# Performance work log

Measured on AMD Instinct MI355X. Metric: run time of the kernel, lower is better.

Reference implementation:

```python
import jax, jax.numpy as jnp
import numpy as np

B = 2          # number of point clouds (batch vector has B blocks)
N_PER = 16384  # points per cloud
F = 32         # input feature dim
D = 3          # coordinate dim
RATIO = 0.25
R = 0.2        # ball-query radius
K = 64         # max_neighbors
H1 = 64        # MLP hidden
COUT = 128     # MLP output
M = int(N_PER * RATIO)  # centroids per cloud


def setup_inputs() -> dict:
    key = jax.random.key(0)
    k0, k1, k2, k3 = jax.random.split(key, 4)
    x = jax.random.normal(k0, (B * N_PER, F), jnp.float32)
    pos = jax.random.uniform(k1, (B * N_PER, D), jnp.float32)
    batch = jnp.repeat(jnp.arange(B), N_PER)
    W1 = jax.random.normal(k2, (F + D, H1), jnp.float32) / np.sqrt(F + D)
    b1 = jnp.zeros((H1,), jnp.float32)
    W2 = jax.random.normal(k3, (H1, COUT), jnp.float32) / np.sqrt(H1)
    b2 = jnp.zeros((COUT,), jnp.float32)
    return {"x": x, "pos": pos, "batch": batch, "W1": W1, "b1": b1, "W2": W2, "b2": b2}


def _fps(pos_b):
    """Iterative farthest point sampling: (N_PER, D) -> (M,) indices."""
    d0 = jnp.sum((pos_b - pos_b[0]) ** 2, axis=-1)  # start at point 0

    def body(d, _):
        i = jnp.argmax(d)
        d = jnp.minimum(d, jnp.sum((pos_b - pos_b[i]) ** 2, axis=-1))
        return d, i

    _, idxs = jax.lax.scan(body, d0, None, length=M - 1)
    return jnp.concatenate([jnp.zeros((1,), idxs.dtype), idxs])


def _set_abstraction(x_b, pos_b, W1, b1, W2, b2):
    idx = _fps(pos_b)            # (M,)
    pc = pos_b[idx]              # centroid positions (M, D)
    # ball query: squared distances centroids -> all points, capped at K neighbors
    d2 = jnp.sum((pc[:, None, :] - pos_b[None, :, :]) ** 2, axis=-1)  # (M, N_PER)
    neg = jnp.where(d2 <= R * R, -d2, -jnp.inf)
    vals, nbr = jax.lax.top_k(neg, K)        # K nearest within radius
    valid = vals > -jnp.inf                  # (M, K)
    xj = x_b[nbr]                            # (M, K, F)
    pj = pos_b[nbr]                          # (M, K, D)
    # faithful to source: msg = pos_j - pos_i / r  (note: pos_i/r, not (pos_j-pos_i)/r)
    msg = jnp.concatenate([xj, pj - pc[:, None, :] / R], axis=-1)  # (M, K, F+D)
    h = jax.nn.relu(msg @ W1 + b1) @ W2 + b2                       # (M, K, COUT)
    h = jnp.where(valid[:, :, None], h, -jnp.inf)
    out = jnp.max(h, axis=1)                 # max aggregation over neighbors
    out = jnp.where(jnp.isfinite(out), out, 0.0)
    return out, pc


def reference(x, pos, batch, W1, b1, W2, b2):
    xb = x.reshape(B, N_PER, F)
    pb = pos.reshape(B, N_PER, D)
    out, pc = jax.vmap(lambda xx, pp: _set_abstraction(xx, pp, W1, b1, W2, b2))(xb, pb)
    batch_out = jnp.repeat(jnp.arange(B, dtype=batch.dtype), M)
    return out.reshape(B * M, COUT), pc.reshape(B * M, D), batch_out
```

## Files before the change

kernel.cpp:

```cpp
#include <hip/hip_runtime.h>
#include <hip/hip_bf16.h>

#define NPTS 16384
#define MCENT 4096
#define BCLD 2
#define FDIM 32
#define H1DIM 64
#define CODIM 128
#define KNBR 64
#define R2CUT 0.04f

__device__ __forceinline__ float d2e(float ax, float ay, float az,
                                     float bx, float by, float bz) {
  float dx = __fsub_rn(ax, bx);
  float dy = __fsub_rn(ay, by);
  float dz = __fsub_rn(az, bz);
  return __fadd_rn(__fadd_rn(__fmul_rn(dx, dx), __fmul_rn(dy, dy)), __fmul_rn(dz, dz));
}

__device__ __forceinline__ int spread3(int v) {
  return ((v & 4) << 4) | ((v & 2) << 2) | (v & 1);
}
__device__ __forceinline__ int cell_of(float x, float y, float z) {
  int cx = min(7, (int)(x * 8.0f));
  int cy = min(7, (int)(y * 8.0f));
  int cz = min(7, (int)(z * 8.0f));
  return (spread3(cx) << 2) | (spread3(cy) << 1) | spread3(cz);
}

#define DPP_LEXMAX_STEP(bb, nn, ctrl)                                          \
  do {                                                                         \
    unsigned _ob = (unsigned)__builtin_amdgcn_update_dpp(0, (int)(bb), ctrl,   \
                                                         0xf, 0xf, false);     \
    unsigned _on = (unsigned)__builtin_amdgcn_update_dpp(0, (int)(nn), ctrl,   \
                                                         0xf, 0xf, false);     \
    bool _t = (_ob > (bb)) || (_ob == (bb) && _on > (nn));                     \
    (bb) = _t ? _ob : (bb);                                                    \
    (nn) = _t ? _on : (nn);                                                    \
  } while (0)

__device__ __forceinline__ int rdlane(int v, int l) {
  return __builtin_amdgcn_readlane(v, l);
}
__device__ __forceinline__ float rdlanef(float v, int l) {
  return __int_as_float(__builtin_amdgcn_readlane(__float_as_int(v), l));
}

__global__ __launch_bounds__(1024) void fps_kernel(const float* __restrict__ pos,
                                                   int* __restrict__ fps_idx,
                                                   float4* __restrict__ ws_sorted) {
  const int b = blockIdx.x;
  const float* P = pos + (size_t)b * NPTS * 3;
  float4* S = ws_sorted + (size_t)b * NPTS;
  const int tid = threadIdx.x;
  const int lane = tid & 63;
  const int wave = tid >> 6;

  __shared__ int hist[512];
  __shared__ int offs[512];
  __shared__ unsigned long long skey[2][16];
  __shared__ float4 spos[2][16];
  __shared__ int winners[MCENT];

  if (tid < 512) hist[tid] = 0;
  __syncthreads();
#pragma unroll 4
  for (int j = 0; j < 16; ++j) {
    int i = tid + j * 1024;
    float x = P[3 * i + 0], y = P[3 * i + 1], z = P[3 * i + 2];
    atomicAdd(&hist[cell_of(x, y, z)], 1);
  }
  __syncthreads();
  if (tid < 64) {
    int base = tid * 8;
    int loc[8];
    int run = 0;
#pragma unroll
    for (int k = 0; k < 8; ++k) { loc[k] = run; run += hist[base + k]; }
    int inc = run;
#pragma unroll
    for (int off = 1; off < 64; off <<= 1) {
      int o = __shfl_up(inc, off);
      if (tid >= off) inc += o;
    }
    int ex = inc - run;
#pragma unroll
    for (int k = 0; k < 8; ++k) offs[base + k] = ex + loc[k];
  }
  __syncthreads();
#pragma unroll 4
  for (int j = 0; j < 16; ++j) {
    int i = tid + j * 1024;
    float x = P[3 * i + 0], y = P[3 * i + 1], z = P[3 * i + 2];
    int p = atomicAdd(&offs[cell_of(x, y, z)], 1);
    S[p] = make_float4(x, y, z, __int_as_float(i));
  }
  __syncthreads();

  float px[16], py[16], pz[16], d[16];
  unsigned nidx[16];
  const float x0 = P[0], y0 = P[1], z0 = P[2];
  float bxm, bxM, bym, byM, bzm, bzM;
  unsigned tb = 0u, tn = 0u;
  float tx = 0.f, ty = 0.f, tz = 0.f;
#pragma unroll
  for (int j = 0; j < 16; ++j) {
    float4 v = S[tid * 16 + j];
    px[j] = v.x; py[j] = v.y; pz[j] = v.z;
    nidx[j] = ~(unsigned)__float_as_int(v.w);
    float dj = d2e(v.x, v.y, v.z, x0, y0, z0);
    d[j] = dj;
    if (j == 0) {
      bxm = v.x; bxM = v.x; bym = v.y; byM = v.y; bzm = v.z; bzM = v.z;
    } else {
      bxm = fminf(bxm, v.x); bxM = fmaxf(bxM, v.x);
      bym = fminf(bym, v.y); byM = fmaxf(byM, v.y);
      bzm = fminf(bzm, v.z); bzM = fmaxf(bzM, v.z);
    }
    unsigned db = __float_as_uint(dj);
    unsigned nj = nidx[j];
    bool t = (db > tb) || (db == tb && nj > tn);
    tb = t ? db : tb; tn = t ? nj : tn;
    tx = t ? v.x : tx; ty = t ? v.y : ty; tz = t ? v.z : tz;
  }

  if (tid == 0) winners[0] = 0;

  bool wavedirty = true;
  unsigned cwb = 0u, cwn = 0u;
  float cwx = 0.f, cwy = 0.f, cwz = 0.f;

  for (int m = 1; m < MCENT; ++m) {
    const int par = m & 1;

    if (wavedirty) {
      unsigned bb = tb, nn = tn;
      DPP_LEXMAX_STEP(bb, nn, 0x111);
      DPP_LEXMAX_STEP(bb, nn, 0x112);
      DPP_LEXMAX_STEP(bb, nn, 0x114);
      DPP_LEXMAX_STEP(bb, nn, 0x118);
      DPP_LEXMAX_STEP(bb, nn, 0x142);
      DPP_LEXMAX_STEP(bb, nn, 0x143);
      cwb = (unsigned)rdlane((int)bb, 63);
      cwn = (unsigned)rdlane((int)nn, 63);
      unsigned long long own = __ballot(tb == cwb && tn == cwn);
      int ol = (int)__ffsll(own) - 1;
      cwx = rdlanef(tx, ol);
      cwy = rdlanef(ty, ol);
      cwz = rdlanef(tz, ol);
    }
    if (lane == 0) {
      skey[par][wave] = ((unsigned long long)cwb << 32) | (unsigned long long)cwn;
      spos[par][wave] = make_float4(cwx, cwy, cwz, 0.0f);
    }
    __syncthreads();

    unsigned rb, rn;
    unsigned sb0 = 0u, sn0 = 0u;
    {
      unsigned bb = 0u, nn = 0u;
      if (lane < 16) {
        unsigned long long kk = skey[par][lane];
        bb = (unsigned)(kk >> 32);
        nn = (unsigned)kk;
        sb0 = bb; sn0 = nn;
        DPP_LEXMAX_STEP(bb, nn, 0x111);
        DPP_LEXMAX_STEP(bb, nn, 0x112);
        DPP_LEXMAX_STEP(bb, nn, 0x114);
        DPP_LEXMAX_STEP(bb, nn, 0x118);
      }
      rb = (unsigned)rdlane((int)bb, 15);
      rn = (unsigned)rdlane((int)nn, 15);
    }
    unsigned long long wm = __ballot(lane < 16 && sb0 == rb && sn0 == rn);
    int ws = (int)__ffsll(wm) - 1;
    float4 wp = spos[par][ws];
    if (tid == 0) winners[m] = (int)(~rn);

    float ex = fmaxf(fmaxf(bxm - wp.x, wp.x - bxM), 0.0f);
    float ey = fmaxf(fmaxf(bym - wp.y, wp.y - byM), 0.0f);
    float ez = fmaxf(fmaxf(bzm - wp.z, wp.z - bzM), 0.0f);
    float lb = (ex * ex + ey * ey + ez * ez) * 0.999f;
    bool mydirty = lb < __uint_as_float(tb);
    if (mydirty) {
      unsigned nb = 0u, nn2 = 0u;
      float nx = 0.f, ny = 0.f, nz = 0.f;
#pragma unroll
      for (int j = 0; j < 16; ++j) {
        float dj = fminf(d[j], d2e(px[j], py[j], pz[j], wp.x, wp.y, wp.z));
        d[j] = dj;
        unsigned db = __float_as_uint(dj);
        unsigned nj = nidx[j];
        bool t = (db > nb) || (db == nb && nj > nn2);
        nb = t ? db : nb; nn2 = t ? nj : nn2;
        nx = t ? px[j] : nx; ny = t ? py[j] : ny; nz = t ? pz[j] : nz;
      }
      tb = nb; tn = nn2; tx = nx; ty = ny; tz = nz;
    }
    wavedirty = (__ballot(mydirty) != 0ULL);
  }

  __syncthreads();
  for (int i = tid; i < MCENT; i += 1024) fps_idx[b * MCENT + i] = winners[i];
}

__global__ __launch_bounds__(256) void ballq_kernel(const float* __restrict__ pos,
                                                    const int* __restrict__ fps_idx,
                                                    int* __restrict__ nbr,
                                                    float* __restrict__ out_pc,
                                                    float* __restrict__ out_batch) {
  const int wave = threadIdx.x >> 6;
  const int lane = threadIdx.x & 63;
  const int c = blockIdx.x * 4 + wave;
  const int b = c >> 12;
  const float* P = pos + (size_t)b * NPTS * 3;

  const int ci = fps_idx[c];
  const float cx = P[3 * ci + 0];
  const float cy = P[3 * ci + 1];
  const float cz = P[3 * ci + 2];
  if (lane == 0) {
    out_pc[3 * c + 0] = cx;
    out_pc[3 * c + 1] = cy;
    out_pc[3 * c + 2] = cz;
    out_batch[c] = (float)b;
  }

  __shared__ unsigned long long list[4][1024];
  __shared__ int cnt[4];
  if (lane == 0) cnt[wave] = 0;

  for (int i = lane; i < NPTS; i += 64) {
    const float qx = P[3 * i + 0];
    const float qy = P[3 * i + 1];
    const float qz = P[3 * i + 2];
    const float dd = d2e(cx, cy, cz, qx, qy, qz);
    if (dd <= R2CUT) {
      int p = atomicAdd(&cnt[wave], 1);
      if (p < 1024)
        list[wave][p] = ((unsigned long long)__float_as_uint(dd) << 32)
                      | (unsigned long long)(unsigned)i;
    }
  }
  __syncthreads();

  int n = cnt[wave];
  if (n > 1024) n = 1024;

  unsigned long long loc[16];
#pragma unroll
  for (int k = 0; k < 16; ++k) {
    int i = lane + k * 64;
    loc[k] = (i < n) ? list[wave][i] : ~0ULL;
  }
  unsigned long long mv = loc[0];
#pragma unroll
  for (int k = 1; k < 16; ++k)
    if (loc[k] < mv) mv = loc[k];

  int myout = -1;
  for (int s = 0; s < 64; ++s) {
    unsigned long long wmin = mv;
#pragma unroll
    for (int off = 32; off >= 1; off >>= 1) {
      unsigned long long o = __shfl_xor(wmin, off);
      if (o < wmin) wmin = o;
    }
    if (lane == s) myout = (wmin == ~0ULL) ? -1 : (int)(unsigned)wmin;
    if (mv == wmin && wmin != ~0ULL) {
#pragma unroll
      for (int k = 0; k < 16; ++k)
        if (loc[k] == wmin) loc[k] = ~0ULL;
      mv = loc[0];
#pragma unroll
      for (int k = 1; k < 16; ++k)
        if (loc[k] < mv) mv = loc[k];
    }
  }
  nbr[c * KNBR + lane] = myout;
}

__global__ __launch_bounds__(256) void mlp_kernel(const float* __restrict__ pos,
                                                  const float* __restrict__ x,
                                                  const int* __restrict__ fps_idx,
                                                  const int* __restrict__ nbr,
                                                  const float* __restrict__ W1,
                                                  const float* __restrict__ b1,
                                                  const float* __restrict__ W2,
                                                  const float* __restrict__ b2,
                                                  float* __restrict__ out) {
  const int c = blockIdx.x;
  const int b = c >> 12;
  const float* P = pos + (size_t)b * NPTS * 3;
  const float* X = x + (size_t)b * NPTS * FDIM;

  __shared__ float W1s[35 * 64];
  __shared__ float W2s[64 * 128];
  __shared__ float b1s[64];
  __shared__ float b2s[128];
  __shared__ float h1s[64][64];
  __shared__ float pmax[2][128];
  __shared__ int validk[64];

  const int tid = threadIdx.x;
  for (int i = tid; i < 35 * 64; i += 256) W1s[i] = W1[i];
  for (int i = tid; i < 64 * 128; i += 256) W2s[i] = W2[i];
  if (tid < 64) b1s[tid] = b1[tid];
  else if (tid < 192) b2s[tid - 64] = b2[tid - 64];

  const int ci = fps_idx[c];
  const float c5x = P[3 * ci + 0] / 0.2f;
  const float c5y = P[3 * ci + 1] / 0.2f;
  const float c5z = P[3 * ci + 2] / 0.2f;

  const int k = tid >> 2, q = tid & 3;
  const int nk = nbr[c * KNBR + k];
  if (q == 0) validk[k] = (nk >= 0) ? 1 : 0;
  const int nkc = (nk < 0) ? 0 : nk;

  float msg[35];
  const float4* Xr = (const float4*)(X + (size_t)nkc * FDIM);
#pragma unroll
  for (int i4 = 0; i4 < 8; ++i4) {
    float4 v = Xr[i4];
    msg[i4 * 4 + 0] = v.x; msg[i4 * 4 + 1] = v.y;
    msg[i4 * 4 + 2] = v.z; msg[i4 * 4 + 3] = v.w;
  }
  msg[32] = P[3 * nkc + 0] - c5x;
  msg[33] = P[3 * nkc + 1] - c5y;
  msg[34] = P[3 * nkc + 2] - c5z;

  __syncthreads();

  float acc[16];
#pragma unroll
  for (int h = 0; h < 16; ++h) acc[h] = b1s[q * 16 + h];
#pragma unroll
  for (int i = 0; i < 35; ++i) {
    const float m = msg[i];
    const float4* wrow = (const float4*)&W1s[i * 64 + q * 16];
#pragma unroll
    for (int j4 = 0; j4 < 4; ++j4) {
      float4 w = wrow[j4];
      acc[j4 * 4 + 0] += m * w.x;
      acc[j4 * 4 + 1] += m * w.y;
      acc[j4 * 4 + 2] += m * w.z;
      acc[j4 * 4 + 3] += m * w.w;
    }
  }
#pragma unroll
  for (int h = 0; h < 16; ++h) h1s[k][q * 16 + h] = fmaxf(acc[h], 0.0f);
  __syncthreads();

  const int ch = tid & 127, half = tid >> 7;
  float w2r[64];
#pragma unroll
  for (int i = 0; i < 64; ++i) w2r[i] = W2s[i * 128 + ch];

  float mx = -INFINITY;
  for (int k2 = half * 32; k2 < half * 32 + 32; ++k2) {
    if (!validk[k2]) continue;
    float s = b2s[ch];
    const float4* hr = (const float4*)h1s[k2];
#pragma unroll
    for (int i4 = 0; i4 < 16; ++i4) {
      float4 h4 = hr[i4];
      s += h4.x * w2r[i4 * 4 + 0] + h4.y * w2r[i4 * 4 + 1]
         + h4.z * w2r[i4 * 4 + 2] + h4.w * w2r[i4 * 4 + 3];
    }
    mx = fmaxf(mx, s);
  }
  pmax[half][ch] = mx;
  __syncthreads();

  if (tid < 128) {
    float m2 = fmaxf(pmax[0][tid], pmax[1][tid]);
    out[(size_t)c * CODIM + tid] = (m2 > -INFINITY) ? m2 : 0.0f;
  }
}

extern "C" void kernel_launch(void* const* d_in, const int* in_sizes, int n_in,
                              void* d_out, int out_size, void* d_ws, size_t ws_size,
                              hipStream_t stream) {
  const float* x   = (const float*)d_in[0];
  const float* pos = (const float*)d_in[1];
  const float* W1  = (const float*)d_in[3];
  const float* b1  = (const float*)d_in[4];
  const float* W2  = (const float*)d_in[5];
  const float* b2  = (const float*)d_in[6];
  float* out = (float*)d_out;

  int* fps_idx = (int*)d_ws;
  int* nbr     = (int*)d_ws + BCLD * MCENT;
  float4* ws_sorted = (float4*)nbr;

  float* out_pc    = out + (size_t)BCLD * MCENT * CODIM;
  float* out_batch = out_pc + (size_t)BCLD * MCENT * 3;

  hipLaunchKernelGGL(fps_kernel, dim3(BCLD), dim3(1024), 0, stream, pos, fps_idx, ws_sorted);
  hipLaunchKernelGGL(ballq_kernel, dim3(BCLD * MCENT / 4), dim3(256), 0, stream,
                     pos, fps_idx, nbr, out_pc, out_batch);
  hipLaunchKernelGGL(mlp_kernel, dim3(BCLD * MCENT), dim3(256), 0, stream,
                     pos, x, fps_idx, nbr, W1, b1, W2, b2, out);
}
```

Before: 7.694 ms.

## Halve FPS block size with 32 points per thread and per-half bounding boxes

```diff
diff --git a/kernel.cpp b/kernel.cpp
--- a/kernel.cpp
+++ b/kernel.cpp
@@ -46,9 +46,9 @@
   return __int_as_float(__builtin_amdgcn_readlane(__float_as_int(v), l));
 }
 
-__global__ __launch_bounds__(1024) void fps_kernel(const float* __restrict__ pos,
-                                                   int* __restrict__ fps_idx,
-                                                   float4* __restrict__ ws_sorted) {
+__global__ __launch_bounds__(512, 2) void fps_kernel(const float* __restrict__ pos,
+                                                     int* __restrict__ fps_idx,
+                                                     float4* __restrict__ ws_sorted) {
   const int b = blockIdx.x;
   const float* P = pos + (size_t)b * NPTS * 3;
   float4* S = ws_sorted + (size_t)b * NPTS;
@@ -58,15 +58,15 @@
 
   __shared__ int hist[512];
   __shared__ int offs[512];
-  __shared__ unsigned long long skey[2][16];
-  __shared__ float4 spos[2][16];
+  __shared__ unsigned long long skey[2][8];
+  __shared__ float4 spos[2][8];
   __shared__ int winners[MCENT];
 
-  if (tid < 512) hist[tid] = 0;
+  hist[tid] = 0;
   __syncthreads();
 #pragma unroll 4
-  for (int j = 0; j < 16; ++j) {
-    int i = tid + j * 1024;
+  for (int j = 0; j < 32; ++j) {
+    int i = tid + j * 512;
     float x = P[3 * i + 0], y = P[3 * i + 1], z = P[3 * i + 2];
     atomicAdd(&hist[cell_of(x, y, z)], 1);
   }
@@ -89,39 +89,47 @@
   }
   __syncthreads();
 #pragma unroll 4
-  for (int j = 0; j < 16; ++j) {
-    int i = tid + j * 1024;
+  for (int j = 0; j < 32; ++j) {
+    int i = tid + j * 512;
     float x = P[3 * i + 0], y = P[3 * i + 1], z = P[3 * i + 2];
     int p = atomicAdd(&offs[cell_of(x, y, z)], 1);
     S[p] = make_float4(x, y, z, __int_as_float(i));
   }
   __syncthreads();
 
-  float px[16], py[16], pz[16], d[16];
-  unsigned nidx[16];
+  float px[32], py[32], pz[32], d[32];
+  unsigned nidx[32];
+  float bxm[2], bxM[2], bym[2], byM[2], bzm[2], bzM[2];
+  unsigned hb[2], hn[2];
+  float hx[2], hy[2], hz[2];
   const float x0 = P[0], y0 = P[1], z0 = P[2];
-  float bxm, bxM, bym, byM, bzm, bzM;
-  unsigned tb = 0u, tn = 0u;
-  float tx = 0.f, ty = 0.f, tz = 0.f;
-#pragma unroll
-  for (int j = 0; j < 16; ++j) {
-    float4 v = S[tid * 16 + j];
-    px[j] = v.x; py[j] = v.y; pz[j] = v.z;
-    nidx[j] = ~(unsigned)__float_as_int(v.w);
-    float dj = d2e(v.x, v.y, v.z, x0, y0, z0);
-    d[j] = dj;
-    if (j == 0) {
-      bxm = v.x; bxM = v.x; bym = v.y; byM = v.y; bzm = v.z; bzM = v.z;
-    } else {
-      bxm = fminf(bxm, v.x); bxM = fmaxf(bxM, v.x);
-      bym = fminf(bym, v.y); byM = fmaxf(byM, v.y);
-      bzm = fminf(bzm, v.z); bzM = fmaxf(bzM, v.z);
-    }
-    unsigned db = __float_as_uint(dj);
-    unsigned nj = nidx[j];
-    bool t = (db > tb) || (db == tb && nj > tn);
-    tb = t ? db : tb; tn = t ? nj : tn;
-    tx = t ? v.x : tx; ty = t ? v.y : ty; tz = t ? v.z : tz;
+#pragma unroll
+  for (int h = 0; h < 2; ++h) {
+    unsigned nb = 0u, nn2 = 0u;
+    float nx = 0.f, ny = 0.f, nz = 0.f;
+#pragma unroll
+    for (int jj = 0; jj < 16; ++jj) {
+      const int j = h * 16 + jj;
+      float4 v = S[tid * 32 + j];
+      px[j] = v.x; py[j] = v.y; pz[j] = v.z;
+      nidx[j] = ~(unsigned)__float_as_int(v.w);
+      float dj = d2e(v.x, v.y, v.z, x0, y0, z0);
+      d[j] = dj;
+      if (jj == 0) {
+        bxm[h] = v.x; bxM[h] = v.x; bym[h] = v.y; byM[h] = v.y;
+        bzm[h] = v.z; bzM[h] = v.z;
+      } else {
+        bxm[h] = fminf(bxm[h], v.x); bxM[h] = fmaxf(bxM[h], v.x);
+        bym[h] = fminf(bym[h], v.y); byM[h] = fmaxf(byM[h], v.y);
+        bzm[h] = fminf(bzm[h], v.z); bzM[h] = fmaxf(bzM[h], v.z);
+      }
+      unsigned db = __float_as_uint(dj);
+      unsigned nj = nidx[j];
+      bool t = (db > nb) || (db == nb && nj > nn2);
+      nb = t ? db : nb; nn2 = t ? nj : nn2;
+      nx = t ? v.x : nx; ny = t ? v.y : ny; nz = t ? v.z : nz;
+    }
+    hb[h] = nb; hn[h] = nn2; hx[h] = nx; hy[h] = ny; hz[h] = nz;
   }
 
   if (tid == 0) winners[0] = 0;
@@ -132,6 +140,14 @@
 
   for (int m = 1; m < MCENT; ++m) {
     const int par = m & 1;
+
+    unsigned tb = hb[0], tn = hn[0];
+    float tx = hx[0], ty = hy[0], tz = hz[0];
+    {
+      bool t = (hb[1] > tb) || (hb[1] == tb && hn[1] > tn);
+      tb = t ? hb[1] : tb; tn = t ? hn[1] : tn;
+      tx = t ? hx[1] : tx; ty = t ? hy[1] : ty; tz = t ? hz[1] : tz;
+    }
 
     if (wavedirty) {
       unsigned bb = tb, nn = tn;
@@ -159,7 +175,7 @@
     unsigned sb0 = 0u, sn0 = 0u;
     {
       unsigned bb = 0u, nn = 0u;
-      if (lane < 16) {
+      if (lane < 8) {
         unsigned long long kk = skey[par][lane];
         bb = (unsigned)(kk >> 32);
         nn = (unsigned)kk;
@@ -167,41 +183,45 @@
         DPP_LEXMAX_STEP(bb, nn, 0x111);
         DPP_LEXMAX_STEP(bb, nn, 0x112);
         DPP_LEXMAX_STEP(bb, nn, 0x114);
-        DPP_LEXMAX_STEP(bb, nn, 0x118);
       }
-      rb = (unsigned)rdlane((int)bb, 15);
-      rn = (unsigned)rdlane((int)nn, 15);
-    }
-    unsigned long long wm = __ballot(lane < 16 && sb0 == rb && sn0 == rn);
+      rb = (unsigned)rdlane((int)bb, 7);
+      rn = (unsigned)rdlane((int)nn, 7);
+    }
+    unsigned long long wm = __ballot(lane < 8 && sb0 == rb && sn0 == rn);
     int ws = (int)__ffsll(wm) - 1;
     float4 wp = spos[par][ws];
     if (tid == 0) winners[m] = (int)(~rn);
 
-    float ex = fmaxf(fmaxf(bxm - wp.x, wp.x - bxM), 0.0f);
-    float ey = fmaxf(fmaxf(bym - wp.y, wp.y - byM), 0.0f);
-    float ez = fmaxf(fmaxf(bzm - wp.z, wp.z - bzM), 0.0f);
-    float lb = (ex * ex + ey * ey + ez * ez) * 0.999f;
-    bool mydirty = lb < __uint_as_float(tb);
-    if (mydirty) {
-      unsigned nb = 0u, nn2 = 0u;
-      float nx = 0.f, ny = 0.f, nz = 0.f;
-#pragma unroll
-      for (int j = 0; j < 16; ++j) {
-        float dj = fminf(d[j], d2e(px[j], py[j], pz[j], wp.x, wp.y, wp.z));
-        d[j] = dj;
-        unsigned db = __float_as_uint(dj);
-        unsigned nj = nidx[j];
-        bool t = (db > nb) || (db == nb && nj > nn2);
-        nb = t ? db : nb; nn2 = t ? nj : nn2;
-        nx = t ? px[j] : nx; ny = t ? py[j] : ny; nz = t ? pz[j] : nz;
+    bool mydirty = false;
+#pragma unroll
+    for (int h = 0; h < 2; ++h) {
+      float ex = fmaxf(fmaxf(bxm[h] - wp.x, wp.x - bxM[h]), 0.0f);
+      float ey = fmaxf(fmaxf(bym[h] - wp.y, wp.y - byM[h]), 0.0f);
+      float ez = fmaxf(fmaxf(bzm[h] - wp.z, wp.z - bzM[h]), 0.0f);
+      float lb = (ex * ex + ey * ey + ez * ez) * 0.999f;
+      if (lb < __uint_as_float(hb[h])) {
+        mydirty = true;
+        unsigned nb = 0u, nn2 = 0u;
+        float nx = 0.f, ny = 0.f, nz = 0.f;
+#pragma unroll
+        for (int jj = 0; jj < 16; ++jj) {
+          const int j = h * 16 + jj;
+          float dj = fminf(d[j], d2e(px[j], py[j], pz[j], wp.x, wp.y, wp.z));
+          d[j] = dj;
+          unsigned db = __float_as_uint(dj);
+          unsigned nj = nidx[j];
+          bool t = (db > nb) || (db == nb && nj > nn2);
+          nb = t ? db : nb; nn2 = t ? nj : nn2;
+          nx = t ? px[j] : nx; ny = t ? py[j] : ny; nz = t ? pz[j] : nz;
+        }
+        hb[h] = nb; hn[h] = nn2; hx[h] = nx; hy[h] = ny; hz[h] = nz;
       }
-      tb = nb; tn = nn2; tx = nx; ty = ny; tz = nz;
     }
     wavedirty = (__ballot(mydirty) != 0ULL);
   }
 
   __syncthreads();
-  for (int i = tid; i < MCENT; i += 1024) fps_idx[b * MCENT + i] = winners[i];
+  for (int i = tid; i < MCENT; i += 512) fps_idx[b * MCENT + i] = winners[i];
 }
 
 __global__ __launch_bounds__(256) void ballq_kernel(const float* __restrict__ pos,
@@ -397,7 +417,7 @@
   float* out_pc    = out + (size_t)BCLD * MCENT * CODIM;
   float* out_batch = out_pc + (size_t)BCLD * MCENT * 3;
 
-  hipLaunchKernelGGL(fps_kernel, dim3(BCLD), dim3(1024), 0, stream, pos, fps_idx, ws_sorted);
+  hipLaunchKernelGGL(fps_kernel, dim3(BCLD), dim3(512), 0, stream, pos, fps_idx, ws_sorted);
   hipLaunchKernelGGL(ballq_kernel, dim3(BCLD * MCENT / 4), dim3(256), 0, stream,
                      pos, fps_idx, nbr, out_pc, out_batch);
   hipLaunchKernelGGL(mlp_kernel, dim3(BCLD * MCENT), dim3(256), 0, stream,
```

New measurement: 11.39 ms. 1.48x slower.
